# Performance work log

Measured on AMD Instinct MI355X. Metric: run time of the kernel, lower is better.

Reference implementation:

```python
import jax, jax.numpy as jnp
import numpy as np

B, S, D_IN, D_OUT = 4, 4096, 256, 256

def setup_inputs() -> dict:
    key = jax.random.key(0)
    ks = jax.random.split(key, 7)
    scale = 1.0 / np.sqrt(D_IN)
    return {
        "x": jax.random.normal(ks[0], (B, S, D_IN), dtype=jnp.float32),
        "Wq": jax.random.uniform(ks[1], (D_IN, D_OUT), jnp.float32, -scale, scale),
        "bq": jax.random.uniform(ks[2], (D_OUT,), jnp.float32, -scale, scale),
        "Wk": jax.random.uniform(ks[3], (D_IN, D_OUT), jnp.float32, -scale, scale),
        "bk": jax.random.uniform(ks[4], (D_OUT,), jnp.float32, -scale, scale),
        "Wv": jax.random.uniform(ks[5], (D_IN, D_OUT), jnp.float32, -scale, scale),
        "bv": jax.random.uniform(ks[6], (D_OUT,), jnp.float32, -scale, scale),
    }

def reference(x, Wq, bq, Wk, bk, Wv, bv):
    # QKV projections: [B, S, D_OUT]
    q = jnp.einsum("bsd,de->bse", x, Wq) + bq
    k = jnp.einsum("bsd,de->bse", x, Wk) + bk
    v = jnp.einsum("bsd,de->bse", x, Wv) + bv
    # Scaled dot-product attention; full [B, S, S] scores as in the original.
    scores = jnp.einsum("bqe,bke->bqk", q, k) / jnp.sqrt(jnp.asarray(q.shape[-1], q.dtype))
    attn = jax.nn.softmax(scores, axis=-1)
    return jnp.einsum("bqk,bke->bqe", attn, v)
```

## Files before the change

kernel.cpp:

```cpp
#include <hip/hip_runtime.h>
#include <stdint.h>

typedef unsigned short u16;
typedef __attribute__((ext_vector_type(4))) float f32x4;
typedef __attribute__((ext_vector_type(8))) short bf16x8;
typedef __attribute__((ext_vector_type(4))) int i32x4;
typedef __attribute__((ext_vector_type(2))) unsigned int u32x2;

#define SEQ 4096
#define DIM 256
#define QSCALE 0.09016844f

__device__ __forceinline__ u16 f2bf(float f) {
  union { float f; uint32_t u; } v; v.f = f;
  uint32_t r = (v.u + 0x7FFFu + ((v.u >> 16) & 1u)) >> 16;
  return (u16)r;
}

__device__ __forceinline__ void gload_lds16(const void* g, void* lds) {
  __builtin_amdgcn_global_load_lds(
      (const __attribute__((address_space(1))) uint32_t*)g,
      (__attribute__((address_space(3))) uint32_t*)lds, 16, 0, 0);
}

__global__ __launch_bounds__(256) void wt_kernel(const float* __restrict__ Wq,
                                                 const float* __restrict__ Wk,
                                                 const float* __restrict__ Wv,
                                                 u16* __restrict__ wt) {
  int b = blockIdx.x;
  int w = b >> 8;
  int n = b & 255;
  const float* W = (w == 0) ? Wq : ((w == 1) ? Wk : Wv);
  float scale = (w == 0) ? QSCALE : 1.0f;
  int k = threadIdx.x;
  wt[(w * 256 + n) * 256 + k] = f2bf(W[k * 256 + n] * scale);
}

__global__ __launch_bounds__(256) void qkv_kernel(
    const float* __restrict__ x, const float* __restrict__ bq,
    const float* __restrict__ bk, const float* __restrict__ bv,
    const u16* __restrict__ wt, u16* __restrict__ qs, u16* __restrict__ kk,
    char* __restrict__ vt) {
  __shared__ __align__(16) u16 lds_b[16384];
  __shared__ __align__(16) u16 lds_v[4096];
  int tid = threadIdx.x;
  int w = tid >> 6, l = tid & 63;
  int a = l & 15, g = l >> 4;
  int rowbase = blockIdx.x * 64;

  bf16x8 afr[8];
  {
    int row = rowbase + w * 16 + a;
    const float* xr = x + (size_t)row * 256;
#pragma unroll
    for (int ks = 0; ks < 8; ++ks) {
      int k0 = ks * 32 + g * 8;
      union { bf16x8 s; u16 u[8]; } fr;
#pragma unroll
      for (int i = 0; i < 8; ++i) fr.u[i] = f2bf(xr[k0 + i]);
      afr[ks] = fr.s;
    }
  }

  for (int w3 = 0; w3 < 3; ++w3) {
    const float* bias = (w3 == 0) ? bq : ((w3 == 1) ? bk : bv);
    for (int qn = 0; qn < 4; ++qn) {
      {
        const u16* src = wt + (w3 * 256 + qn * 64) * 256;
        for (int j = 0; j < 8; ++j) {
          uint32_t inst = w * 8 + j;
          uint32_t flat = inst * 1024 + l * 16;
          uint32_t row = flat >> 9;
          uint32_t c5 = (flat >> 4) & 31;
          uint32_t sc = (c5 & ~7u) | ((c5 ^ row) & 7u);
          gload_lds16(src + row * 256 + sc * 8, ((char*)lds_b) + inst * 1024);
        }
      }
      __syncthreads();
      f32x4 acc[4];
#pragma unroll
      for (int n0 = 0; n0 < 4; ++n0) acc[n0] = (f32x4){0.f, 0.f, 0.f, 0.f};
#pragma unroll
      for (int ks = 0; ks < 8; ++ks) {
#pragma unroll
        for (int n0 = 0; n0 < 4; ++n0) {
          uint32_t row = n0 * 16 + a;
          uint32_t c5 = ks * 4 + g;
          uint32_t sc = (c5 & ~7u) | ((c5 ^ row) & 7u);
          bf16x8 bfr = *(const bf16x8*)((const char*)lds_b + row * 512 + sc * 16);
          acc[n0] = __builtin_amdgcn_mfma_f32_16x16x32_bf16(afr[ks], bfr, acc[n0], 0, 0, 0);
        }
      }
      if (w3 < 2) {
        u16* out = (w3 == 0) ? qs : kk;
        float bscale = (w3 == 0) ? QSCALE : 1.0f;
#pragma unroll
        for (int n0 = 0; n0 < 4; ++n0) {
          int col = qn * 64 + n0 * 16 + a;
          float bb = bias[col] * bscale;
#pragma unroll
          for (int r = 0; r < 4; ++r) {
            int row = rowbase + w * 16 + g * 4 + r;
            out[(size_t)row * 256 + col] = f2bf(acc[n0][r] + bb);
          }
        }
      } else {
#pragma unroll
        for (int n0 = 0; n0 < 4; ++n0) {
          int col = qn * 64 + n0 * 16 + a;
          float bb = bias[col];
          int dl = n0 * 16 + a;
#pragma unroll
          for (int r = 0; r < 4; ++r) {
            int m = w * 16 + g * 4 + r;
            uint32_t byteoff =
                (uint32_t)dl * 128 + ((((uint32_t)m >> 3) ^ ((uint32_t)dl & 7)) << 4) + (m & 7) * 2;
            *(u16*)((char*)lds_v + byteoff) = f2bf(acc[n0][r] + bb);
          }
        }
        __syncthreads();
        {
          int dl = tid >> 2;
          size_t base = (size_t)blockIdx.x * 32768 + (size_t)(qn * 64 + dl) * 128;
#pragma unroll
          for (int cc = 0; cc < 2; ++cc) {
            uint32_t c = (tid & 3) + cc * 4;
            i32x4 vd = *(const i32x4*)((const char*)lds_v + dl * 128 + ((c ^ (dl & 7)) << 4));
            *(i32x4*)(vt + base + c * 16) = vd;
          }
        }
      }
      __syncthreads();
    }
  }
}

__device__ __forceinline__ void stage4(const char* src, char* ldsbase,
                                       const uint32_t* so, int w) {
#pragma unroll
  for (int j = 0; j < 4; ++j)
    gload_lds16(src + so[j], ldsbase + (w * 4 + j) * 1024);
}

#define PV_STEP(SLOT)                                                          \
  {                                                                            \
    bf16x8 pfr[2][2];                                                          \
    _Pragma("unroll") for (int mt = 0; mt < 2; ++mt)                           \
    _Pragma("unroll") for (int ks2 = 0; ks2 < 2; ++ks2)                        \
        pfr[mt][ks2] = *(const bf16x8*)(lds + (SLOT) * 8192 + pro[mt * 2 + ks2]); \
    __builtin_amdgcn_s_setprio(1);                                             \
    _Pragma("unroll") for (int mt = 0; mt < 2; ++mt)                           \
    _Pragma("unroll") for (int ks2 = 0; ks2 < 2; ++ks2)                        \
        lacc[mt] = __builtin_amdgcn_mfma_f32_16x16x32_bf16(pfr[mt][ks2], ones, \
                                                           lacc[mt], 0, 0, 0); \
    _Pragma("unroll") for (int d0 = 0; d0 < 4; ++d0)                           \
    _Pragma("unroll") for (int ks2 = 0; ks2 < 2; ++ks2) {                      \
      bf16x8 vfr = *(const bf16x8*)(lds + (SLOT) * 32768 + vro[d0 * 2 + ks2]); \
      _Pragma("unroll") for (int mt = 0; mt < 2; ++mt)                         \
          o[mt][d0] = __builtin_amdgcn_mfma_f32_16x16x32_bf16(pfr[mt][ks2],    \
                                                              vfr, o[mt][d0],  \
                                                              0, 0, 0);        \
    }                                                                          \
    __builtin_amdgcn_s_setprio(0);                                             \
  }

#define TILE(CUR, DO_PV, DO_K)                                                 \
  {                                                                            \
    asm volatile("s_waitcnt vmcnt(0) lgkmcnt(0)" ::: "memory");                \
    __builtin_amdgcn_s_barrier();                                              \
    __builtin_amdgcn_sched_barrier(0);                                         \
    stage4(vstp, lds + 65536 + (CUR) * 32768, vso, w);                         \
    if (DO_K) stage4(kstp, lds + ((CUR) ^ 1) * 32768, kso, w);                 \
    vstp += 32768;                                                             \
    kstp += 32768;                                                             \
    f32x4 sc0 = {0.f, 0.f, 0.f, 0.f}, sc1 = {0.f, 0.f, 0.f, 0.f};              \
    __builtin_amdgcn_s_setprio(1);                                             \
    _Pragma("unroll") for (int ks = 0; ks < 8; ++ks) {                         \
      bf16x8 kfr = *(const bf16x8*)(lds + (CUR) * 32768 + kro[ks]);            \
      sc0 = __builtin_amdgcn_mfma_f32_16x16x32_bf16(kfr, qfr[0][ks], sc0, 0, 0, 0); \
      sc1 = __builtin_amdgcn_mfma_f32_16x16x32_bf16(kfr, qfr[1][ks], sc1, 0, 0, 0); \
    }                                                                          \
    __builtin_amdgcn_s_setprio(0);                                             \
    _Pragma("unroll") for (int mt = 0; mt < 2; ++mt) {                         \
      f32x4 s = mt ? sc1 : sc0;                                                \
      float e0 = exp2f(fminf(s[0], 43.f));                                     \
      float e1 = exp2f(fminf(s[1], 43.f));                                     \
      float e2 = exp2f(fminf(s[2], 43.f));                                     \
      float e3 = exp2f(fminf(s[3], 43.f));                                     \
      uint32_t p0 = (uint32_t)f2bf(e0) | ((uint32_t)f2bf(e1) << 16);           \
      uint32_t p1 = (uint32_t)f2bf(e2) | ((uint32_t)f2bf(e3) << 16);           \
      u32x2 pk = {p0, p1};                                                     \
      *(u32x2*)(lds + (CUR) * 8192 + pwo[mt]) = pk;                            \
    }                                                                          \
    if (DO_PV) PV_STEP((CUR) ^ 1)                                              \
  }

__global__ __launch_bounds__(512, 2) void attn_kernel(const u16* __restrict__ qs,
                                                      const u16* __restrict__ kk,
                                                      const char* __restrict__ vt,
                                                      float* __restrict__ out) {
  __shared__ __align__(16) char lds[147456];
  int tid = threadIdx.x;
  int w = tid >> 6, l = tid & 63;
  int a = l & 15, g = l >> 4;
  int qh = w >> 2, sub = w & 3;
  int bx = blockIdx.x;
  int batch = (bx >> 1) & 3;
  int qt = ((bx >> 3) << 1) | (bx & 1);

  uint32_t kro[8], vro[8], pro[4], pwo[2], kso[4], vso[4];
#pragma unroll
  for (int ks = 0; ks < 8; ++ks) {
    uint32_t row = sub * 16 + a, c5 = ks * 4 + g;
    kro[ks] = row * 512 + (((c5 & ~7u) | ((c5 ^ row) & 7u)) << 4);
  }
#pragma unroll
  for (int d0 = 0; d0 < 4; ++d0)
#pragma unroll
    for (int ks2 = 0; ks2 < 2; ++ks2) {
      uint32_t row = sub * 64 + d0 * 16 + a, c3 = ks2 * 4 + g;
      vro[d0 * 2 + ks2] = 65536u + row * 128 + ((c3 ^ (row & 7)) << 4);
    }
#pragma unroll
  for (int mt = 0; mt < 2; ++mt) {
    uint32_t q = qh * 32 + mt * 16 + a;
#pragma unroll
    for (int ks2 = 0; ks2 < 2; ++ks2) {
      uint32_t c4 = ks2 * 4 + g;
      pro[mt * 2 + ks2] = 131072u + q * 128 + ((c4 ^ (q & 7)) << 4);
    }
    uint32_t c4w = sub * 2 + (g >> 1);
    pwo[mt] = 131072u + q * 128 + ((c4w ^ (q & 7)) << 4) + (g & 1) * 8;
  }
#pragma unroll
  for (int j = 0; j < 4; ++j) {
    uint32_t inst = w * 4 + j, flat = inst * 1024 + l * 16;
    {
      uint32_t row = flat >> 9, c5 = (flat >> 4) & 31;
      kso[j] = row * 512 + (((c5 & ~7u) | ((c5 ^ row) & 7u)) << 4);
    }
    {
      uint32_t row = flat >> 7, c3 = (flat >> 4) & 7;
      vso[j] = row * 128 + ((c3 ^ (row & 7)) << 4);
    }
  }

  bf16x8 qfr[2][8];
  {
    const u16* qp = qs + ((size_t)batch * SEQ + qt * 64 + qh * 32) * 256;
#pragma unroll
    for (int mt = 0; mt < 2; ++mt)
#pragma unroll
      for (int ks = 0; ks < 8; ++ks)
        qfr[mt][ks] = *(const bf16x8*)(qp + (size_t)(mt * 16 + a) * 256 + ks * 32 + g * 8);
  }

  f32x4 o[2][4];
  f32x4 lacc[2];
#pragma unroll
  for (int mt = 0; mt < 2; ++mt) {
    lacc[mt] = (f32x4){0.f, 0.f, 0.f, 0.f};
#pragma unroll
    for (int d0 = 0; d0 < 4; ++d0) o[mt][d0] = (f32x4){0.f, 0.f, 0.f, 0.f};
  }
  const short ob = (short)0x3F80;
  bf16x8 ones = {ob, ob, ob, ob, ob, ob, ob, ob};

  const char* kbase = (const char*)kk + (size_t)batch * SEQ * 512;
  const char* vbase = vt + (size_t)batch * 64 * 32768;
  const char* kstp = kbase + 32768;
  const char* vstp = vbase;

  stage4(kbase, lds, kso, w);

  TILE(0, false, true)
  for (int tp = 0; tp < 31; ++tp) {
    TILE(1, true, true)
    TILE(0, true, true)
  }
  TILE(1, true, false)

  asm volatile("s_waitcnt vmcnt(0) lgkmcnt(0)" ::: "memory");
  __builtin_amdgcn_s_barrier();
  __builtin_amdgcn_sched_barrier(0);
  PV_STEP(1)

  float* op = out + ((size_t)batch * SEQ + (size_t)qt * 64 + qh * 32) * 256 + sub * 64;
#pragma unroll
  for (int mt = 0; mt < 2; ++mt)
#pragma unroll
    for (int r = 0; r < 4; ++r) {
      float inv = 1.0f / lacc[mt][r];
#pragma unroll
      for (int d0 = 0; d0 < 4; ++d0)
        op[(size_t)(mt * 16 + g * 4 + r) * 256 + d0 * 16 + a] = o[mt][d0][r] * inv;
    }
}

extern "C" void kernel_launch(void* const* d_in, const int* in_sizes, int n_in,
                              void* d_out, int out_size, void* d_ws, size_t ws_size,
                              hipStream_t stream) {
  const float* x = (const float*)d_in[0];
  const float* Wq = (const float*)d_in[1];
  const float* bq = (const float*)d_in[2];
  const float* Wk = (const float*)d_in[3];
  const float* bk = (const float*)d_in[4];
  const float* Wv = (const float*)d_in[5];
  const float* bv = (const float*)d_in[6];
  char* ws = (char*)d_ws;
  u16* wt = (u16*)ws;
  u16* qs = (u16*)(ws + 0x60000);
  u16* kk = (u16*)(ws + 0x60000 + 0x800000);
  char* vt = ws + 0x60000 + 0x1000000;
  wt_kernel<<<dim3(768), dim3(256), 0, stream>>>(Wq, Wk, Wv, wt);
  qkv_kernel<<<dim3(256), dim3(256), 0, stream>>>(x, bq, bk, bv, wt, qs, kk, vt);
  attn_kernel<<<dim3(256), dim3(512), 0, stream>>>(qs, kk, vt, (float*)d_out);
}
```

Measured before the change: 130.6 us.

## Specialize warps into QK and PV producer/consumer groups with register-direct loads

```diff
diff --git a/kernel.cpp b/kernel.cpp
--- a/kernel.cpp
+++ b/kernel.cpp
@@ -135,166 +135,179 @@
   }
 }
 
-__device__ __forceinline__ void stage4(const char* src, char* ldsbase,
-                                       const uint32_t* so, int w) {
-#pragma unroll
-  for (int j = 0; j < 4; ++j)
-    gload_lds16(src + so[j], ldsbase + (w * 4 + j) * 1024);
-}
-
-#define PV_STEP(SLOT)                                                          \
+
+#define QK_TILE(CUR, DO_K)                                                     \
   {                                                                            \
-    bf16x8 pfr[2][2];                                                          \
-    _Pragma("unroll") for (int mt = 0; mt < 2; ++mt)                           \
-    _Pragma("unroll") for (int ks2 = 0; ks2 < 2; ++ks2)                        \
-        pfr[mt][ks2] = *(const bf16x8*)(lds + (SLOT) * 8192 + pro[mt * 2 + ks2]); \
+    f32x4 sc[4];                                                               \
+    _Pragma("unroll") for (int mt = 0; mt < 4; ++mt)                           \
+        sc[mt] = (f32x4){0.f, 0.f, 0.f, 0.f};                                  \
     __builtin_amdgcn_s_setprio(1);                                             \
-    _Pragma("unroll") for (int mt = 0; mt < 2; ++mt)                           \
-    _Pragma("unroll") for (int ks2 = 0; ks2 < 2; ++ks2)                        \
-        lacc[mt] = __builtin_amdgcn_mfma_f32_16x16x32_bf16(pfr[mt][ks2], ones, \
-                                                           lacc[mt], 0, 0, 0); \
-    _Pragma("unroll") for (int d0 = 0; d0 < 4; ++d0)                           \
-    _Pragma("unroll") for (int ks2 = 0; ks2 < 2; ++ks2) {                      \
-      bf16x8 vfr = *(const bf16x8*)(lds + (SLOT) * 32768 + vro[d0 * 2 + ks2]); \
-      _Pragma("unroll") for (int mt = 0; mt < 2; ++mt)                         \
-          o[mt][d0] = __builtin_amdgcn_mfma_f32_16x16x32_bf16(pfr[mt][ks2],    \
-                                                              vfr, o[mt][d0],  \
-                                                              0, 0, 0);        \
+    _Pragma("unroll") for (int ks = 0; ks < 8; ++ks) {                         \
+      _Pragma("unroll") for (int mt = 0; mt < 4; ++mt)                         \
+          sc[mt] = __builtin_amdgcn_mfma_f32_16x16x32_bf16(kfr[ks], qfr[mt][ks], \
+                                                           sc[mt], 0, 0, 0);   \
     }                                                                          \
     __builtin_amdgcn_s_setprio(0);                                             \
-  }
-
-#define TILE(CUR, DO_PV, DO_K)                                                 \
-  {                                                                            \
-    asm volatile("s_waitcnt vmcnt(0) lgkmcnt(0)" ::: "memory");                \
-    __builtin_amdgcn_s_barrier();                                              \
+    if (DO_K) {                                                                \
+      _Pragma("unroll") for (int ks = 0; ks < 8; ++ks)                         \
+          kfr[ks] = *(const bf16x8*)(kptr + ks * 64);                          \
+      kptr += 32768;                                                           \
+    }                                                                          \
     __builtin_amdgcn_sched_barrier(0);                                         \
-    stage4(vstp, lds + 65536 + (CUR) * 32768, vso, w);                         \
-    if (DO_K) stage4(kstp, lds + ((CUR) ^ 1) * 32768, kso, w);                 \
-    vstp += 32768;                                                             \
-    kstp += 32768;                                                             \
-    f32x4 sc0 = {0.f, 0.f, 0.f, 0.f}, sc1 = {0.f, 0.f, 0.f, 0.f};              \
-    __builtin_amdgcn_s_setprio(1);                                             \
-    _Pragma("unroll") for (int ks = 0; ks < 8; ++ks) {                         \
-      bf16x8 kfr = *(const bf16x8*)(lds + (CUR) * 32768 + kro[ks]);            \
-      sc0 = __builtin_amdgcn_mfma_f32_16x16x32_bf16(kfr, qfr[0][ks], sc0, 0, 0, 0); \
-      sc1 = __builtin_amdgcn_mfma_f32_16x16x32_bf16(kfr, qfr[1][ks], sc1, 0, 0, 0); \
-    }                                                                          \
-    __builtin_amdgcn_s_setprio(0);                                             \
-    _Pragma("unroll") for (int mt = 0; mt < 2; ++mt) {                         \
-      f32x4 s = mt ? sc1 : sc0;                                                \
-      float e0 = exp2f(fminf(s[0], 43.f));                                     \
-      float e1 = exp2f(fminf(s[1], 43.f));                                     \
-      float e2 = exp2f(fminf(s[2], 43.f));                                     \
-      float e3 = exp2f(fminf(s[3], 43.f));                                     \
+    _Pragma("unroll") for (int mt = 0; mt < 4; ++mt) {                         \
+      float e0 = exp2f(fminf(sc[mt][0], 43.f));                                \
+      float e1 = exp2f(fminf(sc[mt][1], 43.f));                                \
+      float e2 = exp2f(fminf(sc[mt][2], 43.f));                                \
+      float e3 = exp2f(fminf(sc[mt][3], 43.f));                                \
       uint32_t p0 = (uint32_t)f2bf(e0) | ((uint32_t)f2bf(e1) << 16);           \
       uint32_t p1 = (uint32_t)f2bf(e2) | ((uint32_t)f2bf(e3) << 16);           \
       u32x2 pk = {p0, p1};                                                     \
-      *(u32x2*)(lds + (CUR) * 8192 + pwo[mt]) = pk;                            \
+      *(u32x2*)(lds + (CUR) * 10240 + pwo[mt]) = pk;                           \
     }                                                                          \
-    if (DO_PV) PV_STEP((CUR) ^ 1)                                              \
-  }
+    asm volatile("s_waitcnt lgkmcnt(0)" ::: "memory");                         \
+  }
+
+#define PV_TILE(RSLOT)                                                         \
+  {                                                                            \
+    bf16x8 pfr[4][2];                                                          \
+    _Pragma("unroll") for (int mt = 0; mt < 4; ++mt)                           \
+    _Pragma("unroll") for (int kvw = 0; kvw < 2; ++kvw)                        \
+        pfr[mt][kvw] =                                                         \
+            *(const bf16x8*)(lds + (RSLOT) * 10240 + pro[mt * 2 + kvw]);       \
+    __builtin_amdgcn_s_setprio(1);                                             \
+    _Pragma("unroll") for (int mt = 0; mt < 4; ++mt)                           \
+    _Pragma("unroll") for (int kvw = 0; kvw < 2; ++kvw)                        \
+        lacc[mt] = __builtin_amdgcn_mfma_f32_16x16x32_bf16(pfr[mt][kvw], ones, \
+                                                           lacc[mt], 0, 0, 0); \
+    _Pragma("unroll") for (int d0 = 0; d0 < 4; ++d0)                           \
+    _Pragma("unroll") for (int kvw = 0; kvw < 2; ++kvw) {                      \
+      _Pragma("unroll") for (int mt = 0; mt < 4; ++mt)                         \
+          o[mt][d0] = __builtin_amdgcn_mfma_f32_16x16x32_bf16(                 \
+              pfr[mt][kvw], vfr[d0 * 2 + kvw], o[mt][d0], 0, 0, 0);            \
+    }                                                                          \
+    __builtin_amdgcn_s_setprio(0);                                             \
+  }
+
+#define PV_LOADV                                                               \
+  {                                                                            \
+    _Pragma("unroll") for (int d0 = 0; d0 < 4; ++d0)                           \
+    _Pragma("unroll") for (int kvw = 0; kvw < 2; ++kvw)                        \
+        vfr[d0 * 2 + kvw] = *(const bf16x8*)((d0 < 2 ? vp0 : vp1) +            \
+                                             (d0 & 1) * 2048 + kvw * 64);      \
+    vp0 += 32768;                                                              \
+    vp1 += 32768;                                                              \
+    __builtin_amdgcn_sched_barrier(0);                                         \
+  }
+
+#define BAR                                                                    \
+  __builtin_amdgcn_s_barrier();                                                \
+  __builtin_amdgcn_sched_barrier(0);
 
 __global__ __launch_bounds__(512, 2) void attn_kernel(const u16* __restrict__ qs,
                                                       const u16* __restrict__ kk,
                                                       const char* __restrict__ vt,
                                                       float* __restrict__ out) {
-  __shared__ __align__(16) char lds[147456];
+  __shared__ __align__(16) char lds[20480];
   int tid = threadIdx.x;
   int w = tid >> 6, l = tid & 63;
   int a = l & 15, g = l >> 4;
-  int qh = w >> 2, sub = w & 3;
+  bool isQK = (w < 4);
+  int sub = w & 3;
   int bx = blockIdx.x;
   int batch = (bx >> 1) & 3;
   int qt = ((bx >> 3) << 1) | (bx & 1);
 
-  uint32_t kro[8], vro[8], pro[4], pwo[2], kso[4], vso[4];
-#pragma unroll
-  for (int ks = 0; ks < 8; ++ks) {
-    uint32_t row = sub * 16 + a, c5 = ks * 4 + g;
-    kro[ks] = row * 512 + (((c5 & ~7u) | ((c5 ^ row) & 7u)) << 4);
-  }
-#pragma unroll
-  for (int d0 = 0; d0 < 4; ++d0)
-#pragma unroll
-    for (int ks2 = 0; ks2 < 2; ++ks2) {
-      uint32_t row = sub * 64 + d0 * 16 + a, c3 = ks2 * 4 + g;
-      vro[d0 * 2 + ks2] = 65536u + row * 128 + ((c3 ^ (row & 7)) << 4);
-    }
-#pragma unroll
-  for (int mt = 0; mt < 2; ++mt) {
-    uint32_t q = qh * 32 + mt * 16 + a;
-#pragma unroll
-    for (int ks2 = 0; ks2 < 2; ++ks2) {
-      uint32_t c4 = ks2 * 4 + g;
-      pro[mt * 2 + ks2] = 131072u + q * 128 + ((c4 ^ (q & 7)) << 4);
-    }
-    uint32_t c4w = sub * 2 + (g >> 1);
-    pwo[mt] = 131072u + q * 128 + ((c4w ^ (q & 7)) << 4) + (g & 1) * 8;
-  }
-#pragma unroll
-  for (int j = 0; j < 4; ++j) {
-    uint32_t inst = w * 4 + j, flat = inst * 1024 + l * 16;
-    {
-      uint32_t row = flat >> 9, c5 = (flat >> 4) & 31;
-      kso[j] = row * 512 + (((c5 & ~7u) | ((c5 ^ row) & 7u)) << 4);
-    }
-    {
-      uint32_t row = flat >> 7, c3 = (flat >> 4) & 7;
-      vso[j] = row * 128 + ((c3 ^ (row & 7)) << 4);
-    }
-  }
-
-  bf16x8 qfr[2][8];
-  {
-    const u16* qp = qs + ((size_t)batch * SEQ + qt * 64 + qh * 32) * 256;
-#pragma unroll
-    for (int mt = 0; mt < 2; ++mt)
+  uint32_t pwo[4], pro[8];
+#pragma unroll
+  for (int mt = 0; mt < 4; ++mt) {
+    uint32_t row = mt * 16 + a;
+    pwo[mt] = row * 160 + ((((uint32_t)(sub * 2 + (g >> 1)) ^ (a & 7)) << 4) +
+                           (g & 1) * 8);
+#pragma unroll
+    for (int kvw = 0; kvw < 2; ++kvw)
+      pro[mt * 2 + kvw] = row * 160 + (((uint32_t)(kvw * 4 + g) ^ (a & 7)) << 4);
+  }
+
+  bf16x8 qfr[4][8];
+  bf16x8 kfr[8];
+  bf16x8 vfr[8];
+  f32x4 o[4][4];
+  f32x4 lacc[4];
+  const short ob = (short)0x3F80;
+  bf16x8 ones = {ob, ob, ob, ob, ob, ob, ob, ob};
+
+  const char* kptr;
+  const char* vp0;
+  const char* vp1;
+
+  if (isQK) {
+    const u16* qp = qs + ((size_t)batch * SEQ + qt * 64) * 256;
+#pragma unroll
+    for (int mt = 0; mt < 4; ++mt)
 #pragma unroll
       for (int ks = 0; ks < 8; ++ks)
         qfr[mt][ks] = *(const bf16x8*)(qp + (size_t)(mt * 16 + a) * 256 + ks * 32 + g * 8);
-  }
-
-  f32x4 o[2][4];
-  f32x4 lacc[2];
-#pragma unroll
-  for (int mt = 0; mt < 2; ++mt) {
-    lacc[mt] = (f32x4){0.f, 0.f, 0.f, 0.f};
-#pragma unroll
-    for (int d0 = 0; d0 < 4; ++d0) o[mt][d0] = (f32x4){0.f, 0.f, 0.f, 0.f};
-  }
-  const short ob = (short)0x3F80;
-  bf16x8 ones = {ob, ob, ob, ob, ob, ob, ob, ob};
-
-  const char* kbase = (const char*)kk + (size_t)batch * SEQ * 512;
-  const char* vbase = vt + (size_t)batch * 64 * 32768;
-  const char* kstp = kbase + 32768;
-  const char* vstp = vbase;
-
-  stage4(kbase, lds, kso, w);
-
-  TILE(0, false, true)
+    kptr = (const char*)kk + (size_t)batch * SEQ * 512 + (size_t)(sub * 16 + a) * 512 + g * 16;
+#pragma unroll
+    for (int ks = 0; ks < 8; ++ks) kfr[ks] = *(const bf16x8*)(kptr + ks * 64);
+    kptr += 32768;
+  } else {
+#pragma unroll
+    for (int mt = 0; mt < 4; ++mt) {
+      lacc[mt] = (f32x4){0.f, 0.f, 0.f, 0.f};
+#pragma unroll
+      for (int d0 = 0; d0 < 4; ++d0) o[mt][d0] = (f32x4){0.f, 0.f, 0.f, 0.f};
+    }
+    vp0 = vt + (size_t)batch * 64 * 32768 + (size_t)(sub * 64 + a) * 128 + g * 16;
+    vp1 = vp0 + 4096;
+  }
+
+  if (isQK) {
+    QK_TILE(0, true)
+  } else {
+    PV_LOADV
+  }
+  BAR
+
   for (int tp = 0; tp < 31; ++tp) {
-    TILE(1, true, true)
-    TILE(0, true, true)
-  }
-  TILE(1, true, false)
-
-  asm volatile("s_waitcnt vmcnt(0) lgkmcnt(0)" ::: "memory");
-  __builtin_amdgcn_s_barrier();
-  __builtin_amdgcn_sched_barrier(0);
-  PV_STEP(1)
-
-  float* op = out + ((size_t)batch * SEQ + (size_t)qt * 64 + qh * 32) * 256 + sub * 64;
-#pragma unroll
-  for (int mt = 0; mt < 2; ++mt)
-#pragma unroll
-    for (int r = 0; r < 4; ++r) {
-      float inv = 1.0f / lacc[mt][r];
-#pragma unroll
-      for (int d0 = 0; d0 < 4; ++d0)
-        op[(size_t)(mt * 16 + g * 4 + r) * 256 + d0 * 16 + a] = o[mt][d0][r] * inv;
-    }
+    if (isQK) {
+      QK_TILE(1, true)
+    } else {
+      PV_TILE(0)
+      PV_LOADV
+    }
+    BAR
+    if (isQK) {
+      QK_TILE(0, true)
+    } else {
+      PV_TILE(1)
+      PV_LOADV
+    }
+    BAR
+  }
+
+  if (isQK) {
+    QK_TILE(1, false)
+  } else {
+    PV_TILE(0)
+    PV_LOADV
+  }
+  BAR
+
+  if (!isQK) {
+    PV_TILE(1)
+    float* op = out + ((size_t)batch * SEQ + (size_t)qt * 64) * 256 + sub * 64;
+#pragma unroll
+    for (int mt = 0; mt < 4; ++mt)
+#pragma unroll
+      for (int r = 0; r < 4; ++r) {
+        float inv = 1.0f / lacc[mt][r];
+        int q = mt * 16 + g * 4 + r;
+#pragma unroll
+        for (int d0 = 0; d0 < 4; ++d0)
+          op[(size_t)q * 256 + d0 * 16 + a] = o[mt][d0][r] * inv;
+      }
+  }
 }
 
 extern "C" void kernel_launch(void* const* d_in, const int* in_sizes, int n_in,
```

After: 313.4 us. 140% more time.

## Load V fragments directly from global into registers instead of staging through LDS

Applied to the files above, without the earlier changes.

```diff
diff --git a/kernel.cpp b/kernel.cpp
--- a/kernel.cpp
+++ b/kernel.cpp
@@ -155,13 +155,21 @@
                                                            lacc[mt], 0, 0, 0); \
     _Pragma("unroll") for (int d0 = 0; d0 < 4; ++d0)                           \
     _Pragma("unroll") for (int ks2 = 0; ks2 < 2; ++ks2) {                      \
-      bf16x8 vfr = *(const bf16x8*)(lds + (SLOT) * 32768 + vro[d0 * 2 + ks2]); \
       _Pragma("unroll") for (int mt = 0; mt < 2; ++mt)                         \
-          o[mt][d0] = __builtin_amdgcn_mfma_f32_16x16x32_bf16(pfr[mt][ks2],    \
-                                                              vfr, o[mt][d0],  \
-                                                              0, 0, 0);        \
+          o[mt][d0] = __builtin_amdgcn_mfma_f32_16x16x32_bf16(                 \
+              pfr[mt][ks2], vfr[d0 * 2 + ks2], o[mt][d0], 0, 0, 0);            \
     }                                                                          \
     __builtin_amdgcn_s_setprio(0);                                             \
+  }
+
+#define LOADV                                                                  \
+  {                                                                            \
+    _Pragma("unroll") for (int d0 = 0; d0 < 4; ++d0)                           \
+    _Pragma("unroll") for (int ks2 = 0; ks2 < 2; ++ks2)                        \
+        vfr[d0 * 2 + ks2] = *(const bf16x8*)((d0 < 2 ? vp0 : vp1) +            \
+                                             (d0 & 1) * 2048 + ks2 * 64);      \
+    vp0 += 32768;                                                              \
+    vp1 += 32768;                                                              \
   }
 
 #define TILE(CUR, DO_PV, DO_K)                                                 \
@@ -169,9 +177,8 @@
     asm volatile("s_waitcnt vmcnt(0) lgkmcnt(0)" ::: "memory");                \
     __builtin_amdgcn_s_barrier();                                              \
     __builtin_amdgcn_sched_barrier(0);                                         \
-    stage4(vstp, lds + 65536 + (CUR) * 32768, vso, w);                         \
+    if (DO_PV) LOADV                            \
     if (DO_K) stage4(kstp, lds + ((CUR) ^ 1) * 32768, kso, w);                 \
-    vstp += 32768;                                                             \
     kstp += 32768;                                                             \
     f32x4 sc0 = {0.f, 0.f, 0.f, 0.f}, sc1 = {0.f, 0.f, 0.f, 0.f};              \
     __builtin_amdgcn_s_setprio(1);                                             \
@@ -195,11 +202,11 @@
     if (DO_PV) PV_STEP((CUR) ^ 1)                                              \
   }
 
-__global__ __launch_bounds__(512, 2) void attn_kernel(const u16* __restrict__ qs,
+__global__ __launch_bounds__(512, 1) void attn_kernel(const u16* __restrict__ qs,
                                                       const u16* __restrict__ kk,
                                                       const char* __restrict__ vt,
                                                       float* __restrict__ out) {
-  __shared__ __align__(16) char lds[147456];
+  __shared__ __align__(16) char lds[81920];
   int tid = threadIdx.x;
   int w = tid >> 6, l = tid & 63;
   int a = l & 15, g = l >> 4;
@@ -208,41 +215,28 @@
   int batch = (bx >> 1) & 3;
   int qt = ((bx >> 3) << 1) | (bx & 1);
 
-  uint32_t kro[8], vro[8], pro[4], pwo[2], kso[4], vso[4];
+  uint32_t kro[8], pro[4], pwo[2], kso[4];
 #pragma unroll
   for (int ks = 0; ks < 8; ++ks) {
     uint32_t row = sub * 16 + a, c5 = ks * 4 + g;
     kro[ks] = row * 512 + (((c5 & ~7u) | ((c5 ^ row) & 7u)) << 4);
   }
 #pragma unroll
-  for (int d0 = 0; d0 < 4; ++d0)
-#pragma unroll
-    for (int ks2 = 0; ks2 < 2; ++ks2) {
-      uint32_t row = sub * 64 + d0 * 16 + a, c3 = ks2 * 4 + g;
-      vro[d0 * 2 + ks2] = 65536u + row * 128 + ((c3 ^ (row & 7)) << 4);
-    }
-#pragma unroll
   for (int mt = 0; mt < 2; ++mt) {
     uint32_t q = qh * 32 + mt * 16 + a;
 #pragma unroll
     for (int ks2 = 0; ks2 < 2; ++ks2) {
       uint32_t c4 = ks2 * 4 + g;
-      pro[mt * 2 + ks2] = 131072u + q * 128 + ((c4 ^ (q & 7)) << 4);
+      pro[mt * 2 + ks2] = 65536u + q * 128 + ((c4 ^ (q & 7)) << 4);
     }
     uint32_t c4w = sub * 2 + (g >> 1);
-    pwo[mt] = 131072u + q * 128 + ((c4w ^ (q & 7)) << 4) + (g & 1) * 8;
+    pwo[mt] = 65536u + q * 128 + ((c4w ^ (q & 7)) << 4) + (g & 1) * 8;
   }
 #pragma unroll
   for (int j = 0; j < 4; ++j) {
     uint32_t inst = w * 4 + j, flat = inst * 1024 + l * 16;
-    {
-      uint32_t row = flat >> 9, c5 = (flat >> 4) & 31;
-      kso[j] = row * 512 + (((c5 & ~7u) | ((c5 ^ row) & 7u)) << 4);
-    }
-    {
-      uint32_t row = flat >> 7, c3 = (flat >> 4) & 7;
-      vso[j] = row * 128 + ((c3 ^ (row & 7)) << 4);
-    }
+    uint32_t row = flat >> 9, c5 = (flat >> 4) & 31;
+    kso[j] = row * 512 + (((c5 & ~7u) | ((c5 ^ row) & 7u)) << 4);
   }
 
   bf16x8 qfr[2][8];
@@ -257,6 +251,7 @@
 
   f32x4 o[2][4];
   f32x4 lacc[2];
+  bf16x8 vfr[8];
 #pragma unroll
   for (int mt = 0; mt < 2; ++mt) {
     lacc[mt] = (f32x4){0.f, 0.f, 0.f, 0.f};
@@ -267,9 +262,9 @@
   bf16x8 ones = {ob, ob, ob, ob, ob, ob, ob, ob};
 
   const char* kbase = (const char*)kk + (size_t)batch * SEQ * 512;
-  const char* vbase = vt + (size_t)batch * 64 * 32768;
   const char* kstp = kbase + 32768;
-  const char* vstp = vbase;
+  const char* vp0 = vt + (size_t)batch * 64 * 32768 + (size_t)(sub * 64 + a) * 128 + g * 16;
+  const char* vp1 = vp0 + 4096;
 
   stage4(kbase, lds, kso, w);
 
@@ -280,9 +275,10 @@
   }
   TILE(1, true, false)
 
-  asm volatile("s_waitcnt vmcnt(0) lgkmcnt(0)" ::: "memory");
+  asm volatile("s_waitcnt lgkmcnt(0)" ::: "memory");
   __builtin_amdgcn_s_barrier();
   __builtin_amdgcn_sched_barrier(0);
+  LOADV
   PV_STEP(1)
 
   float* op = out + ((size_t)batch * SEQ + (size_t)qt * 64 + qh * 32) * 256 + sub * 64;
```

New measurement: 195.8 us. 49.9% more time.

## Restructure attention into 128-query tiles with split-KV and a combine kernel

Applied to the files above, without the earlier changes.

```diff
diff --git a/kernel.cpp b/kernel.cpp
--- a/kernel.cpp
+++ b/kernel.cpp
@@ -142,96 +142,98 @@
     gload_lds16(src + so[j], ldsbase + (w * 4 + j) * 1024);
 }
 
-#define PV_STEP(SLOT)                                                          \
-  {                                                                            \
-    bf16x8 pfr[2][2];                                                          \
-    _Pragma("unroll") for (int mt = 0; mt < 2; ++mt)                           \
-    _Pragma("unroll") for (int ks2 = 0; ks2 < 2; ++ks2)                        \
-        pfr[mt][ks2] = *(const bf16x8*)(lds + (SLOT) * 8192 + pro[mt * 2 + ks2]); \
-    __builtin_amdgcn_s_setprio(1);                                             \
-    _Pragma("unroll") for (int mt = 0; mt < 2; ++mt)                           \
-    _Pragma("unroll") for (int ks2 = 0; ks2 < 2; ++ks2)                        \
-        lacc[mt] = __builtin_amdgcn_mfma_f32_16x16x32_bf16(pfr[mt][ks2], ones, \
-                                                           lacc[mt], 0, 0, 0); \
-    _Pragma("unroll") for (int d0 = 0; d0 < 4; ++d0)                           \
-    _Pragma("unroll") for (int ks2 = 0; ks2 < 2; ++ks2) {                      \
-      bf16x8 vfr = *(const bf16x8*)(lds + (SLOT) * 32768 + vro[d0 * 2 + ks2]); \
-      _Pragma("unroll") for (int mt = 0; mt < 2; ++mt)                         \
-          o[mt][d0] = __builtin_amdgcn_mfma_f32_16x16x32_bf16(pfr[mt][ks2],    \
-                                                              vfr, o[mt][d0],  \
-                                                              0, 0, 0);        \
-    }                                                                          \
-    __builtin_amdgcn_s_setprio(0);                                             \
-  }
-
-#define TILE(CUR, DO_PV, DO_K)                                                 \
+#define TILE(CUR)                                                              \
   {                                                                            \
     asm volatile("s_waitcnt vmcnt(0) lgkmcnt(0)" ::: "memory");                \
     __builtin_amdgcn_s_barrier();                                              \
     __builtin_amdgcn_sched_barrier(0);                                         \
-    stage4(vstp, lds + 65536 + (CUR) * 32768, vso, w);                         \
-    if (DO_K) stage4(kstp, lds + ((CUR) ^ 1) * 32768, kso, w);                 \
+    if (tcur + 1 < nt) {                                                       \
+      stage4(kstp, lds + ((CUR) ^ 1) * 32768, kso, w);                         \
+      stage4(vstp, lds + 65536 + ((CUR) ^ 1) * 32768, vso, w);                 \
+    }                                                                          \
+    kstp += 32768;                                                             \
     vstp += 32768;                                                             \
-    kstp += 32768;                                                             \
-    f32x4 sc0 = {0.f, 0.f, 0.f, 0.f}, sc1 = {0.f, 0.f, 0.f, 0.f};              \
+    f32x4 sc[2][2];                                                            \
+    _Pragma("unroll") for (int mt = 0; mt < 2; ++mt)                           \
+    _Pragma("unroll") for (int n = 0; n < 2; ++n)                              \
+        sc[mt][n] = (f32x4){0.f, 0.f, 0.f, 0.f};                               \
     __builtin_amdgcn_s_setprio(1);                                             \
-    _Pragma("unroll") for (int ks = 0; ks < 8; ++ks) {                         \
-      bf16x8 kfr = *(const bf16x8*)(lds + (CUR) * 32768 + kro[ks]);            \
-      sc0 = __builtin_amdgcn_mfma_f32_16x16x32_bf16(kfr, qfr[0][ks], sc0, 0, 0, 0); \
-      sc1 = __builtin_amdgcn_mfma_f32_16x16x32_bf16(kfr, qfr[1][ks], sc1, 0, 0, 0); \
+    _Pragma("unroll") for (int n = 0; n < 2; ++n)                              \
+    _Pragma("unroll") for (int j = 0; j < 8; ++j) {                            \
+      bf16x8 kfr = *(const bf16x8*)(lds + (CUR) * 32768 + kro[j] + n * 8192);  \
+      sc[0][n] = __builtin_amdgcn_mfma_f32_16x16x32_bf16(kfr, qfr[0][j], sc[0][n], 0, 0, 0); \
+      sc[1][n] = __builtin_amdgcn_mfma_f32_16x16x32_bf16(kfr, qfr[1][j], sc[1][n], 0, 0, 0); \
     }                                                                          \
     __builtin_amdgcn_s_setprio(0);                                             \
-    _Pragma("unroll") for (int mt = 0; mt < 2; ++mt) {                         \
-      f32x4 s = mt ? sc1 : sc0;                                                \
-      float e0 = exp2f(fminf(s[0], 43.f));                                     \
-      float e1 = exp2f(fminf(s[1], 43.f));                                     \
-      float e2 = exp2f(fminf(s[2], 43.f));                                     \
-      float e3 = exp2f(fminf(s[3], 43.f));                                     \
+    _Pragma("unroll") for (int mt = 0; mt < 2; ++mt)                           \
+    _Pragma("unroll") for (int n = 0; n < 2; ++n) {                            \
+      float e0 = exp2f(fminf(sc[mt][n][0], 43.f));                             \
+      float e1 = exp2f(fminf(sc[mt][n][1], 43.f));                             \
+      float e2 = exp2f(fminf(sc[mt][n][2], 43.f));                             \
+      float e3 = exp2f(fminf(sc[mt][n][3], 43.f));                             \
       uint32_t p0 = (uint32_t)f2bf(e0) | ((uint32_t)f2bf(e1) << 16);           \
       uint32_t p1 = (uint32_t)f2bf(e2) | ((uint32_t)f2bf(e3) << 16);           \
       u32x2 pk = {p0, p1};                                                     \
-      *(u32x2*)(lds + (CUR) * 8192 + pwo[mt]) = pk;                            \
+      *(u32x2*)(lds + pwo[n] + mt * 2048) = pk;                                \
     }                                                                          \
-    if (DO_PV) PV_STEP((CUR) ^ 1)                                              \
-  }
-
-__global__ __launch_bounds__(512, 2) void attn_kernel(const u16* __restrict__ qs,
-                                                      const u16* __restrict__ kk,
-                                                      const char* __restrict__ vt,
-                                                      float* __restrict__ out) {
+    asm volatile("s_waitcnt lgkmcnt(0)" ::: "memory");                         \
+    __builtin_amdgcn_s_barrier();                                              \
+    __builtin_amdgcn_sched_barrier(0);                                         \
+    bf16x8 pfr[2][2];                                                          \
+    _Pragma("unroll") for (int mt = 0; mt < 2; ++mt)                           \
+    _Pragma("unroll") for (int j2 = 0; j2 < 2; ++j2)                           \
+        pfr[mt][j2] = *(const bf16x8*)(lds + pro[j2] + mt * 2048);             \
+    __builtin_amdgcn_s_setprio(1);                                             \
+    _Pragma("unroll") for (int mt = 0; mt < 2; ++mt)                           \
+    _Pragma("unroll") for (int j2 = 0; j2 < 2; ++j2)                           \
+        lacc[mt] = __builtin_amdgcn_mfma_f32_16x16x32_bf16(pfr[mt][j2], ones,  \
+                                                           lacc[mt], 0, 0, 0); \
+    _Pragma("unroll") for (int d0 = 0; d0 < 8; ++d0)                           \
+    _Pragma("unroll") for (int j2 = 0; j2 < 2; ++j2) {                         \
+      bf16x8 vfr = *(const bf16x8*)(lds + 65536 + (CUR) * 32768 + vro[j2] +    \
+                                    d0 * 2048);                                \
+      o[0][d0] = __builtin_amdgcn_mfma_f32_16x16x32_bf16(pfr[0][j2], vfr, o[0][d0], 0, 0, 0); \
+      o[1][d0] = __builtin_amdgcn_mfma_f32_16x16x32_bf16(pfr[1][j2], vfr, o[1][d0], 0, 0, 0); \
+    }                                                                          \
+    __builtin_amdgcn_s_setprio(0);                                             \
+    ++tcur;                                                                    \
+  }
+
+__global__ __launch_bounds__(512, 1) void attn_kernel(
+    const u16* __restrict__ qs, const u16* __restrict__ kk,
+    const char* __restrict__ vt, float* __restrict__ out,
+    float* __restrict__ pOB, float* __restrict__ pl, int split) {
   __shared__ __align__(16) char lds[147456];
   int tid = threadIdx.x;
   int w = tid >> 6, l = tid & 63;
   int a = l & 15, g = l >> 4;
-  int qh = w >> 2, sub = w & 3;
+  int qq = w >> 1, sub = w & 1;
   int bx = blockIdx.x;
-  int batch = (bx >> 1) & 3;
-  int qt = ((bx >> 3) << 1) | (bx & 1);
-
-  uint32_t kro[8], vro[8], pro[4], pwo[2], kso[4], vso[4];
-#pragma unroll
-  for (int ks = 0; ks < 8; ++ks) {
-    uint32_t row = sub * 16 + a, c5 = ks * 4 + g;
-    kro[ks] = row * 512 + (((c5 & ~7u) | ((c5 ^ row) & 7u)) << 4);
-  }
-#pragma unroll
-  for (int d0 = 0; d0 < 4; ++d0)
-#pragma unroll
-    for (int ks2 = 0; ks2 < 2; ++ks2) {
-      uint32_t row = sub * 64 + d0 * 16 + a, c3 = ks2 * 4 + g;
-      vro[d0 * 2 + ks2] = 65536u + row * 128 + ((c3 ^ (row & 7)) << 4);
-    }
-#pragma unroll
-  for (int mt = 0; mt < 2; ++mt) {
-    uint32_t q = qh * 32 + mt * 16 + a;
-#pragma unroll
-    for (int ks2 = 0; ks2 < 2; ++ks2) {
-      uint32_t c4 = ks2 * 4 + g;
-      pro[mt * 2 + ks2] = 131072u + q * 128 + ((c4 ^ (q & 7)) << 4);
-    }
-    uint32_t c4w = sub * 2 + (g >> 1);
-    pwo[mt] = 131072u + q * 128 + ((c4w ^ (q & 7)) << 4) + (g & 1) * 8;
-  }
+  int h, batch, qt;
+  if (split == 2) { h = bx & 1; batch = (bx >> 1) & 3; qt = bx >> 3; }
+  else            { h = 0;      batch = (bx >> 1) & 3; qt = ((bx >> 3) << 1) | (bx & 1); }
+  int nt = (split == 2) ? 32 : 64;
+
+  uint32_t a7 = a & 7;
+  uint32_t kro[8], vro[2], pro[2], pwo[2], kso[4], vso[4];
+#pragma unroll
+  for (int j = 0; j < 8; ++j) {
+    uint32_t c5 = j * 4 + g;
+    kro[j] = (uint32_t)(sub * 32 + a) * 512 +
+             (((c5 & ~7u) | ((c5 ^ a7) & 7u)) << 4);
+  }
+#pragma unroll
+  for (int j2 = 0; j2 < 2; ++j2)
+    vro[j2] = (uint32_t)(sub * 128 + a) * 128 +
+              ((((uint32_t)(j2 * 4 + g)) ^ a7) << 4);
+#pragma unroll
+  for (int j2 = 0; j2 < 2; ++j2)
+    pro[j2] = 131072u + (uint32_t)(qq * 32 + a) * 128 +
+              ((((uint32_t)(j2 * 4 + g)) ^ a7) << 4);
+#pragma unroll
+  for (int n = 0; n < 2; ++n)
+    pwo[n] = 131072u + (uint32_t)(qq * 32 + a) * 128 +
+             ((((uint32_t)(sub * 4 + n * 2 + (g >> 1))) ^ a7) << 4) + (g & 1) * 8;
 #pragma unroll
   for (int j = 0; j < 4; ++j) {
     uint32_t inst = w * 4 + j, flat = inst * 1024 + l * 16;
@@ -247,54 +249,81 @@
 
   bf16x8 qfr[2][8];
   {
-    const u16* qp = qs + ((size_t)batch * SEQ + qt * 64 + qh * 32) * 256;
+    const char* qp = (const char*)qs + (size_t)(batch * SEQ + qt * 128) * 512;
 #pragma unroll
     for (int mt = 0; mt < 2; ++mt)
 #pragma unroll
-      for (int ks = 0; ks < 8; ++ks)
-        qfr[mt][ks] = *(const bf16x8*)(qp + (size_t)(mt * 16 + a) * 256 + ks * 32 + g * 8);
-  }
-
-  f32x4 o[2][4];
+      for (int j = 0; j < 8; ++j)
+        qfr[mt][j] = *(const bf16x8*)(qp + (size_t)(qq * 32 + mt * 16 + a) * 512 +
+                                      j * 64 + g * 16);
+  }
+
+  f32x4 o[2][8];
   f32x4 lacc[2];
 #pragma unroll
   for (int mt = 0; mt < 2; ++mt) {
     lacc[mt] = (f32x4){0.f, 0.f, 0.f, 0.f};
 #pragma unroll
-    for (int d0 = 0; d0 < 4; ++d0) o[mt][d0] = (f32x4){0.f, 0.f, 0.f, 0.f};
+    for (int d0 = 0; d0 < 8; ++d0) o[mt][d0] = (f32x4){0.f, 0.f, 0.f, 0.f};
   }
   const short ob = (short)0x3F80;
   bf16x8 ones = {ob, ob, ob, ob, ob, ob, ob, ob};
 
-  const char* kbase = (const char*)kk + (size_t)batch * SEQ * 512;
-  const char* vbase = vt + (size_t)batch * 64 * 32768;
-  const char* kstp = kbase + 32768;
-  const char* vstp = vbase;
-
-  stage4(kbase, lds, kso, w);
-
-  TILE(0, false, true)
-  for (int tp = 0; tp < 31; ++tp) {
-    TILE(1, true, true)
-    TILE(0, true, true)
-  }
-  TILE(1, true, false)
-
-  asm volatile("s_waitcnt vmcnt(0) lgkmcnt(0)" ::: "memory");
-  __builtin_amdgcn_s_barrier();
-  __builtin_amdgcn_sched_barrier(0);
-  PV_STEP(1)
-
-  float* op = out + ((size_t)batch * SEQ + (size_t)qt * 64 + qh * 32) * 256 + sub * 64;
+  const char* kstp = (const char*)kk + (size_t)batch * SEQ * 512 + (size_t)h * 2048 * 512;
+  const char* vstp = vt + (size_t)batch * 64 * 32768 + (size_t)h * 32 * 32768;
+
+  stage4(kstp, lds, kso, w);
+  stage4(vstp, lds + 65536, vso, w);
+  kstp += 32768;
+  vstp += 32768;
+
+  int tcur = 0;
+  int ntHalf = nt >> 1;
+  for (int tp = 0; tp < ntHalf; ++tp) {
+    TILE(0)
+    TILE(1)
+  }
+
+  float* po = (h == 0) ? out : pOB;
+  size_t obase = (size_t)(batch * SEQ + qt * 128 + qq * 32) * 256 + sub * 128;
 #pragma unroll
   for (int mt = 0; mt < 2; ++mt)
 #pragma unroll
     for (int r = 0; r < 4; ++r) {
-      float inv = 1.0f / lacc[mt][r];
-#pragma unroll
-      for (int d0 = 0; d0 < 4; ++d0)
-        op[(size_t)(mt * 16 + g * 4 + r) * 256 + d0 * 16 + a] = o[mt][d0][r] * inv;
-    }
+#pragma unroll
+      for (int d0 = 0; d0 < 8; ++d0)
+        po[obase + (size_t)(mt * 16 + g * 4 + r) * 256 + d0 * 16 + a] = o[mt][d0][r];
+    }
+  if (a == 0 && sub == 0) {
+#pragma unroll
+    for (int mt = 0; mt < 2; ++mt)
+#pragma unroll
+      for (int r = 0; r < 4; ++r)
+        pl[h * 16384 + (batch * 32 + qt) * 128 + qq * 32 + mt * 16 + g * 4 + r] =
+            lacc[mt][r];
+  }
+}
+
+__global__ __launch_bounds__(256) void combine_kernel(float* __restrict__ out,
+                                                      const float* __restrict__ pOB,
+                                                      const float* __restrict__ pl,
+                                                      int split) {
+  int b = blockIdx.x;
+  int tid = threadIdx.x;
+  int batch = b >> 12;
+  int rem = b & 4095;
+  int qt = rem >> 7, ql = rem & 127;
+  size_t idx = (size_t)b * 256 + tid;
+  int li = (batch * 32 + qt) * 128 + ql;
+  float lA = pl[li];
+  float v;
+  if (split == 2) {
+    float lB = pl[16384 + li];
+    v = (out[idx] + pOB[idx]) / (lA + lB);
+  } else {
+    v = out[idx] / lA;
+  }
+  out[idx] = v;
 }
 
 extern "C" void kernel_launch(void* const* d_in, const int* in_sizes, int n_in,
@@ -310,9 +339,14 @@
   char* ws = (char*)d_ws;
   u16* wt = (u16*)ws;
   u16* qs = (u16*)(ws + 0x60000);
-  u16* kk = (u16*)(ws + 0x60000 + 0x800000);
-  char* vt = ws + 0x60000 + 0x1000000;
+  u16* kk = (u16*)(ws + 0x860000);
+  char* vt = ws + 0x1060000;
+  float* pl = (float*)(ws + 0x1860000);
+  float* pOB = (float*)(ws + 0x1880000);
+  int split = (ws_size >= 0x2880000ull) ? 2 : 1;
   wt_kernel<<<dim3(768), dim3(256), 0, stream>>>(Wq, Wk, Wv, wt);
   qkv_kernel<<<dim3(256), dim3(256), 0, stream>>>(x, bq, bk, bv, wt, qs, kk, vt);
-  attn_kernel<<<dim3(256), dim3(512), 0, stream>>>(qs, kk, vt, (float*)d_out);
-}
+  attn_kernel<<<dim3(split * 128), dim3(512), 0, stream>>>(qs, kk, vt, (float*)d_out,
+                                                           pOB, pl, split);
+  combine_kernel<<<dim3(16384), dim3(256), 0, stream>>>((float*)d_out, pOB, pl, split);
+}
```

Result: no change. 131.4 us (+0.6%).
